# Kernel tuning notes

Measured on AMD Instinct MI355X. Metric: run time of the kernel, lower is better.

The kernel has to match this reference:

```python
import jax, jax.numpy as jnp
import numpy as np

N_NODES = 50000
N_EDGES = 800000
IN_DIM = 128
HID = 256
NUM_GRAPHS = 128


def setup_inputs() -> dict:
    key = jax.random.key(0)
    ks = jax.random.split(key, 12)
    x = jax.random.normal(ks[0], (N_NODES, IN_DIM), dtype=jnp.float32)
    edge_index = jax.random.randint(ks[1], (2, N_EDGES), 0, N_NODES, dtype=jnp.int32)
    batch = jnp.sort(jax.random.randint(ks[2], (N_NODES,), 0, NUM_GRAPHS, dtype=jnp.int32))
    def glorot(k, fan_in, fan_out):
        s = jnp.sqrt(6.0 / (fan_in + fan_out))
        return jax.random.uniform(k, (fan_in, fan_out), jnp.float32, -s, s)
    W1 = glorot(ks[3], IN_DIM, HID); b1 = jnp.zeros((HID,), jnp.float32)
    W2 = glorot(ks[4], HID, HID);    b2 = jnp.zeros((HID,), jnp.float32)
    W3 = glorot(ks[5], HID, HID // 2); b3 = jnp.zeros((HID // 2,), jnp.float32)
    W4 = glorot(ks[6], HID // 2, 1);   b4 = jnp.zeros((1,), jnp.float32)
    return {"x": x, "edge_index": edge_index, "batch": batch,
            "W1": W1, "b1": b1, "W2": W2, "b2": b2,
            "W3": W3, "b3": b3, "W4": W4, "b4": b4}


def _gcn_conv(x, src, dst, dinv, W, b, n_nodes):
    # x: [N, F_in] -> [N, F_out]; PyG GCNConv: xW gathered at src, scaled by
    # symmetric norm deg^-1/2[src]*deg^-1/2[dst], scatter-added at dst, + bias.
    h = x @ W                                   # [N, F_out]
    norm = dinv[src] * dinv[dst]                # [E+N]
    msg = h[src] * norm[:, None]                # [E+N, F_out]
    return jax.ops.segment_sum(msg, dst, num_segments=n_nodes) + b


def reference(x, edge_index, batch, W1, b1, W2, b2, W3, b3, W4, b4):
    n = x.shape[0]
    loop = jnp.arange(n, dtype=edge_index.dtype)
    src = jnp.concatenate([edge_index[0], loop])   # add self-loops
    dst = jnp.concatenate([edge_index[1], loop])
    deg = jax.ops.segment_sum(jnp.ones(src.shape[0], x.dtype), dst, num_segments=n)
    dinv = jnp.where(deg > 0, jax.lax.rsqrt(jnp.maximum(deg, 1.0)), 0.0)

    h1 = jax.nn.relu(_gcn_conv(x, src, dst, dinv, W1, b1, n))
    h2 = jax.nn.relu(_gcn_conv(h1, src, dst, dinv, W2, b2, n))

    # global_mean_pool over graph ids
    sums = jax.ops.segment_sum(h2, batch, num_segments=NUM_GRAPHS)          # [G, H]
    cnts = jax.ops.segment_sum(jnp.ones(n, h2.dtype), batch, num_segments=NUM_GRAPHS)
    g = sums / jnp.maximum(cnts, 1.0)[:, None]

    # classifier: Linear->ReLU->(Dropout eval=identity)->Linear->Sigmoid
    z = jax.nn.relu(g @ W3 + b3)
    return jax.nn.sigmoid(z @ W4 + b4)            # [G, 1]
```

## Files before the change

### kernel.cpp

```cpp
#include <hip/hip_runtime.h>
#include <math.h>

#define HID 256
#define INDIM 128
#define NPASS 8

typedef short s16x8 __attribute__((ext_vector_type(8)));
typedef float f32x4 __attribute__((ext_vector_type(4)));
typedef float f32x2 __attribute__((ext_vector_type(2)));

static __device__ __forceinline__ unsigned short f2bf(float f) {
    unsigned int u = __float_as_uint(f);
    unsigned int r = (u + 0x7fffu + ((u >> 16) & 1u)) >> 16;
    return (unsigned short)r;
}

#define DECW(a, base, w)                                                  \
    do {                                                                  \
        f32x2 p0 = __builtin_amdgcn_cvt_pk_f32_fp8((int)(w), false);      \
        f32x2 p1 = __builtin_amdgcn_cvt_pk_f32_fp8((int)(w), true);       \
        a[(base) + 0] += p0[0]; a[(base) + 1] += p0[1];                   \
        a[(base) + 2] += p1[0]; a[(base) + 3] += p1[1];                   \
    } while (0)
#define DEC16(a, u)                                                       \
    do { DECW(a, 0, (u).x); DECW(a, 4, (u).y);                            \
         DECW(a, 8, (u).z); DECW(a, 12, (u).w); } while (0)

__global__ void k_count(const int* __restrict__ dst, int E, int* cnt) {
    int e = blockIdx.x * blockDim.x + threadIdx.x;
    if (e < E) atomicAdd(&cnt[dst[e]], 1);
}

__global__ __launch_bounds__(256) void k_scan_block(const int* __restrict__ cnt,
                                                    int* excl_tmp, int* blksum, int n) {
    __shared__ int sm[256];
    int t = threadIdx.x;
    int i = blockIdx.x * 256 + t;
    int c = (i < n) ? cnt[i] : 0;
    sm[t] = c;
    __syncthreads();
    for (int off = 1; off < 256; off <<= 1) {
        int v = (t >= off) ? sm[t - off] : 0;
        __syncthreads();
        sm[t] += v;
        __syncthreads();
    }
    if (i < n) excl_tmp[i] = sm[t] - c;
    if (t == 255) blksum[blockIdx.x] = sm[255];
}

__global__ __launch_bounds__(256) void k_scan_top(int* blksum, int nb) {
    __shared__ int sm[256];
    int t = threadIdx.x;
    int c = (t < nb) ? blksum[t] : 0;
    sm[t] = c;
    __syncthreads();
    for (int off = 1; off < 256; off <<= 1) {
        int v = (t >= off) ? sm[t - off] : 0;
        __syncthreads();
        sm[t] += v;
        __syncthreads();
    }
    if (t < nb) blksum[t] = sm[t] - c;
}

__global__ __launch_bounds__(256) void k_finalize_rows(const int* __restrict__ excl_tmp,
                                                       const int* __restrict__ blksum,
                                                       const int* __restrict__ cnt,
                                                       int* row_start, int* cursor,
                                                       float* dinv, int n, int E) {
    int i = blockIdx.x * 256 + threadIdx.x;
    if (i < n) {
        int r = excl_tmp[i] + blksum[blockIdx.x];
        row_start[i] = r;
        cursor[i] = r;
        dinv[i] = rsqrtf((float)(cnt[i] + 1));
    }
    if (i == 0) row_start[n] = E;
}

__global__ void k_fill(const int* __restrict__ src, const int* __restrict__ dst,
                       int E, int* cursor, int* __restrict__ csr_src, int n) {
    int e0 = blockIdx.x * blockDim.x + threadIdx.x;
    int stride = gridDim.x * blockDim.x;
    int range = (n + NPASS - 1) / NPASS;
#pragma unroll 1
    for (int p = 0; p < NPASS; p++) {
        int lo = p * range;
        int hi = lo + range;
        for (int e = e0; e < E; e += stride) {
            int d = dst[e];
            if (d >= lo && d < hi) {
                int pos = atomicAdd(&cursor[d], 1);
                csr_src[pos] = src[e];
            }
        }
    }
}

__global__ void k_cast_q(const float* __restrict__ x, const float* __restrict__ dinv,
                         unsigned int* __restrict__ out, int nw) {
    int i = blockIdx.x * blockDim.x + threadIdx.x;
    if (i < nw) {
        float dv = dinv[i >> 5];
        float4 v = ((const float4*)x)[i];
        int w0 = __builtin_amdgcn_cvt_pk_fp8_f32(v.x * dv, v.y * dv, 0, false);
        w0 = __builtin_amdgcn_cvt_pk_fp8_f32(v.z * dv, v.w * dv, w0, true);
        out[i] = (unsigned int)w0;
    }
}

template <int K>
__global__ void k_wt(const float* __restrict__ W, unsigned short* __restrict__ Wt) {
    int c = blockIdx.x;
    int t = threadIdx.x;
    Wt[(size_t)c * K + t] = f2bf(W[(size_t)t * HID + c]);
}

template <int K, int EPI>
__global__ __launch_bounds__(256) void k_gemm_mfma(const unsigned short* __restrict__ Xb,
                                                   const unsigned short* __restrict__ Wt,
                                                   const float* __restrict__ epi,
                                                   void* __restrict__ Yout, int n) {
    constexpr int NK = K / 32;
    const int r0 = blockIdx.x * 32;
    const int w = threadIdx.x >> 6;
    const int lane = threadIdx.x & 63;
    const int ar = lane & 15;
    const int ak = (lane >> 4) * 8;

    int arow[2];
#pragma unroll
    for (int rt = 0; rt < 2; rt++) {
        int r = r0 + rt * 16 + ar;
        arow[rt] = (r < n) ? r : n - 1;
    }
    const unsigned short* Bbase = Wt + (size_t)(w * 64 + ar) * K + ak;

    s16x8 areg[2][NK];
#pragma unroll
    for (int rt = 0; rt < 2; rt++)
#pragma unroll
        for (int kk = 0; kk < NK; kk++)
            areg[rt][kk] = *(const s16x8*)(Xb + (size_t)arow[rt] * K + kk * 32);

    s16x8 breg[4][NK];
#pragma unroll
    for (int ct = 0; ct < 4; ct++)
#pragma unroll
        for (int kk = 0; kk < NK; kk++)
            breg[ct][kk] = *(const s16x8*)(Bbase + (size_t)ct * 16 * K + kk * 32);

    f32x4 acc[2][4];
#pragma unroll
    for (int rt = 0; rt < 2; rt++)
#pragma unroll
        for (int ct = 0; ct < 4; ct++) acc[rt][ct] = f32x4{0, 0, 0, 0};

#pragma unroll
    for (int kk = 0; kk < NK; kk++)
#pragma unroll
        for (int rt = 0; rt < 2; rt++)
#pragma unroll
            for (int ct = 0; ct < 4; ct++)
                acc[rt][ct] = __builtin_amdgcn_mfma_f32_16x16x32_bf16(areg[rt][kk], breg[ct][kk],
                                                                      acc[rt][ct], 0, 0, 0);

#pragma unroll
    for (int rt = 0; rt < 2; rt++) {
        int rbase = r0 + rt * 16 + (lane >> 4) * 4;
        if constexpr (EPI == 1) {
            unsigned short* Yb = (unsigned short*)Yout;
#pragma unroll
            for (int ct = 0; ct < 4; ct++) {
                int c = w * 64 + ct * 16 + ar;
                float bc = epi[c];
#pragma unroll
                for (int j = 0; j < 4; j++) {
                    int r = rbase + j;
                    if (r < n) Yb[(size_t)r * HID + c] = f2bf(fmaxf(acc[rt][ct][j] + bc, 0.0f));
                }
            }
        } else {
            unsigned char* Yq = (unsigned char*)Yout;
            float dv[4];
#pragma unroll
            for (int j = 0; j < 4; j++) dv[j] = (rbase + j < n) ? epi[rbase + j] : 0.0f;
#pragma unroll
            for (int ct = 0; ct < 4; ct++) {
                int c = w * 64 + ct * 16 + ar;
#pragma unroll
                for (int j = 0; j < 4; j++) {
                    int r = rbase + j;
                    if (r < n) {
                        float f = acc[rt][ct][j] * dv[j];
                        int e = __builtin_amdgcn_cvt_pk_fp8_f32(f, f, 0, false);
                        Yq[(size_t)r * HID + c] = (unsigned char)(e & 0xff);
                    }
                }
            }
        }
    }
}

template <int D, bool BIASRELU>
__global__ __launch_bounds__(256) void k_agg_q(const unsigned char* __restrict__ Hq,
                                               const float* __restrict__ dinv,
                                               const int* __restrict__ row_start,
                                               const int* __restrict__ csr_src,
                                               const float* __restrict__ bias,
                                               unsigned short* __restrict__ O, int n) {
    constexpr int LPR = D / 16;
    constexpr int EPW = 64 / LPR;
    const int v = blockIdx.x * 4 + (threadIdx.x >> 6);
    const int lane = threadIdx.x & 63;
    const int sub = lane / LPR;
    const int li = lane % LPR;
    if (v >= n) return;
    const uint4* H4 = (const uint4*)Hq;
    float a[16];
#pragma unroll
    for (int k = 0; k < 16; k++) a[k] = 0.f;
    const int beg = row_start[v], end = row_start[v + 1];
    int i = beg + sub;
    for (; i + 3 * EPW < end; i += 4 * EPW) {
        int s0 = csr_src[i];
        int s1 = csr_src[i + EPW];
        int s2 = csr_src[i + 2 * EPW];
        int s3 = csr_src[i + 3 * EPW];
        uint4 u0 = H4[(size_t)s0 * LPR + li];
        uint4 u1 = H4[(size_t)s1 * LPR + li];
        uint4 u2 = H4[(size_t)s2 * LPR + li];
        uint4 u3 = H4[(size_t)s3 * LPR + li];
        DEC16(a, u0); DEC16(a, u1); DEC16(a, u2); DEC16(a, u3);
    }
    for (; i < end; i += EPW) {
        uint4 u = H4[(size_t)csr_src[i] * LPR + li];
        DEC16(a, u);
    }
#pragma unroll
    for (int off = LPR; off < 64; off <<= 1)
#pragma unroll
        for (int k = 0; k < 16; k++) a[k] += __shfl_xor(a[k], off);

    if (lane < LPR) {
        uint4 us = H4[(size_t)v * LPR + li];
        DEC16(a, us);
        float dv = dinv[v];
        float o[16];
        if constexpr (BIASRELU) {
            const float4* B4 = (const float4*)bias;
#pragma unroll
            for (int q = 0; q < 4; q++) {
                float4 bb = B4[li * 4 + q];
                o[q * 4 + 0] = fmaxf(fmaf(dv, a[q * 4 + 0], bb.x), 0.f);
                o[q * 4 + 1] = fmaxf(fmaf(dv, a[q * 4 + 1], bb.y), 0.f);
                o[q * 4 + 2] = fmaxf(fmaf(dv, a[q * 4 + 2], bb.z), 0.f);
                o[q * 4 + 3] = fmaxf(fmaf(dv, a[q * 4 + 3], bb.w), 0.f);
            }
        } else {
#pragma unroll
            for (int k = 0; k < 16; k++) o[k] = dv * a[k];
        }
        uint4 ow0, ow1;
        ow0.x = (unsigned int)f2bf(o[0]) | ((unsigned int)f2bf(o[1]) << 16);
        ow0.y = (unsigned int)f2bf(o[2]) | ((unsigned int)f2bf(o[3]) << 16);
        ow0.z = (unsigned int)f2bf(o[4]) | ((unsigned int)f2bf(o[5]) << 16);
        ow0.w = (unsigned int)f2bf(o[6]) | ((unsigned int)f2bf(o[7]) << 16);
        ow1.x = (unsigned int)f2bf(o[8]) | ((unsigned int)f2bf(o[9]) << 16);
        ow1.y = (unsigned int)f2bf(o[10]) | ((unsigned int)f2bf(o[11]) << 16);
        ow1.z = (unsigned int)f2bf(o[12]) | ((unsigned int)f2bf(o[13]) << 16);
        ow1.w = (unsigned int)f2bf(o[14]) | ((unsigned int)f2bf(o[15]) << 16);
        uint4* Op = (uint4*)O + (size_t)v * (2 * LPR) + li * 2;
        Op[0] = ow0;
        Op[1] = ow1;
    }
}

#define BFLO(x) __uint_as_float((x) << 16)
#define BFHI(x) __uint_as_float((x) & 0xffff0000u)
#define ACC8(a, u)                                  \
    do {                                            \
        a[0] += BFLO((u).x); a[1] += BFHI((u).x);   \
        a[2] += BFLO((u).y); a[3] += BFHI((u).y);   \
        a[4] += BFLO((u).z); a[5] += BFHI((u).z);   \
        a[6] += BFLO((u).w); a[7] += BFHI((u).w);   \
    } while (0)

__global__ __launch_bounds__(256) void k_pool(const unsigned short* __restrict__ Hb,
                                              const int* __restrict__ batch,
                                              int n, float* __restrict__ G) {
    int g = blockIdx.x;
    int w = threadIdx.x >> 6;
    int lane = threadIdx.x & 63;
    int sub = lane >> 5;
    int li = lane & 31;
    int lo = 0, hi = n;
    while (lo < hi) { int m = (lo + hi) >> 1; if (batch[m] < g) lo = m + 1; else hi = m; }
    int start = lo;
    hi = n;
    while (lo < hi) { int m = (lo + hi) >> 1; if (batch[m] <= g) lo = m + 1; else hi = m; }
    int end = lo;
    const uint4* H4 = (const uint4*)Hb;
    float a[8] = {0, 0, 0, 0, 0, 0, 0, 0};
    for (int v = start + w * 2 + sub; v < end; v += 8) {
        uint4 u = H4[(size_t)v * 32 + li];
        ACC8(a, u);
    }
#pragma unroll
    for (int k = 0; k < 8; k++) a[k] += __shfl_xor(a[k], 32);
    __shared__ float red[4][32][8];
    if (lane < 32) {
#pragma unroll
        for (int k = 0; k < 8; k++) red[w][li][k] = a[k];
    }
    __syncthreads();
    if (w == 0 && lane < 32) {
        float inv = 1.0f / fmaxf((float)(end - start), 1.0f);
        float o[8];
#pragma unroll
        for (int k = 0; k < 8; k++)
            o[k] = (red[0][li][k] + red[1][li][k] + red[2][li][k] + red[3][li][k]) * inv;
        float4* Gp = (float4*)(G + (size_t)g * HID + li * 8);
        Gp[0] = make_float4(o[0], o[1], o[2], o[3]);
        Gp[1] = make_float4(o[4], o[5], o[6], o[7]);
    }
}

__global__ __launch_bounds__(128) void k_cls(const float* __restrict__ G,
                                             const float* __restrict__ W3,
                                             const float* __restrict__ b3,
                                             const float* __restrict__ W4,
                                             const float* __restrict__ b4,
                                             float* __restrict__ out) {
    __shared__ float gr[256];
    __shared__ float red[2];
    int g = blockIdx.x, t = threadIdx.x;
    gr[t] = G[g * 256 + t];
    gr[t + 128] = G[g * 256 + t + 128];
    __syncthreads();
    float z = b3[t];
    for (int k = 0; k < 256; k++) z += gr[k] * W3[k * 128 + t];
    z = fmaxf(z, 0.0f);
    float p = z * W4[t];
    for (int off = 32; off; off >>= 1) p += __shfl_down(p, off);
    if ((t & 63) == 0) red[t >> 6] = p;
    __syncthreads();
    if (t == 0) {
        float tot = red[0] + red[1] + b4[0];
        out[g] = 1.0f / (1.0f + expf(-tot));
    }
}

extern "C" void kernel_launch(void* const* d_in, const int* in_sizes, int n_in,
                              void* d_out, int out_size, void* d_ws, size_t ws_size,
                              hipStream_t stream) {
    const float* x  = (const float*)d_in[0];
    const int*   ei = (const int*)d_in[1];
    const int*   batch = (const int*)d_in[2];
    const float* W1 = (const float*)d_in[3];
    const float* b1 = (const float*)d_in[4];
    const float* W2 = (const float*)d_in[5];
    const float* b2 = (const float*)d_in[6];
    const float* W3 = (const float*)d_in[7];
    const float* b3 = (const float*)d_in[8];
    const float* W4 = (const float*)d_in[9];
    const float* b4 = (const float*)d_in[10];

    const int N = in_sizes[2];
    const int E = in_sizes[1] / 2;
    const int G = out_size;
    const int NB = (N + 255) / 256;

    char* w = (char*)d_ws;
    float* dinv      = (float*)w;  w += ((size_t)N * 4 + 255) & ~(size_t)255;
    int*   cnt       = (int*)w;    w += ((size_t)N * 4 + 255) & ~(size_t)255;
    int*   excl_tmp  = (int*)w;    w += ((size_t)N * 4 + 255) & ~(size_t)255;
    int*   blksum    = (int*)w;    w += 256 * 4;
    int*   row_start = (int*)w;    w += ((size_t)(N + 1) * 4 + 255) & ~(size_t)255;
    int*   cursor    = (int*)w;    w += ((size_t)N * 4 + 255) & ~(size_t)255;
    int*   csr_src   = (int*)w;    w += ((size_t)E * 4 + 255) & ~(size_t)255;
    unsigned char*  xq   = (unsigned char*)w;   w += ((size_t)N * INDIM + 255) & ~(size_t)255;
    unsigned char*  Hq   = (unsigned char*)w;   w += ((size_t)N * HID + 255) & ~(size_t)255;
    unsigned short* w1t  = (unsigned short*)w;  w += ((size_t)INDIM * HID * 2 + 255) & ~(size_t)255;
    unsigned short* w2t  = (unsigned short*)w;  w += ((size_t)HID * HID * 2 + 255) & ~(size_t)255;
    unsigned short* bufA = (unsigned short*)w;  w += (size_t)N * INDIM * 2;
    unsigned short* bufB = (unsigned short*)w;  w += (size_t)N * HID * 2;
    float* gbuf      = (float*)w;  w += (size_t)G * HID * 4;

    const int* src = ei;
    const int* dst = ei + E;

    k_wt<INDIM><<<HID, INDIM, 0, stream>>>(W1, w1t);
    k_wt<HID><<<HID, HID, 0, stream>>>(W2, w2t);

    hipMemsetAsync(cnt, 0, (size_t)N * 4, stream);
    k_count<<<(E + 255) / 256, 256, 0, stream>>>(dst, E, cnt);
    k_scan_block<<<NB, 256, 0, stream>>>(cnt, excl_tmp, blksum, N);
    k_scan_top<<<1, 256, 0, stream>>>(blksum, NB);
    k_finalize_rows<<<NB, 256, 0, stream>>>(excl_tmp, blksum, cnt, row_start, cursor, dinv, N, E);
    k_fill<<<(E + 255) / 256, 256, 0, stream>>>(src, dst, E, cursor, csr_src, N);

    int nw = N * INDIM / 4;
    k_cast_q<<<(nw + 255) / 256, 256, 0, stream>>>(x, dinv, (unsigned int*)xq, nw);

    const int gemm_blocks = (N + 31) / 32;
    const int agg_blocks  = (N + 3) / 4;

    k_agg_q<INDIM, false><<<agg_blocks, 256, 0, stream>>>(xq, dinv, row_start, csr_src, nullptr, bufA, N);
    k_gemm_mfma<INDIM, 1><<<gemm_blocks, 256, 0, stream>>>(bufA, w1t, b1, bufB, N);

    k_gemm_mfma<HID, 2><<<gemm_blocks, 256, 0, stream>>>(bufB, w2t, dinv, Hq, N);
    k_agg_q<HID, true><<<agg_blocks, 256, 0, stream>>>(Hq, dinv, row_start, csr_src, b2, bufB, N);

    k_pool<<<G, 256, 0, stream>>>(bufB, batch, N, gbuf);
    k_cls<<<G, 128, 0, stream>>>(gbuf, W3, b3, W4, b4, (float*)d_out);
}
```

Measured before the change: 296.7 us.

## Stage pre-swizzled weight fragments in LDS and retile GEMM blocks by column

Weights are now pre-packed into the MFMA fragment layout. Each GEMM block loads its 64-column slice of that layout into shared memory once, so waves no longer each fetch a full weight slice from global memory into registers. Blocks now cover 128 rows by 64 columns, with each wave handling 32 rows, and A fragments are prefetched one k-step ahead instead of all being held in registers. This lowers register pressure and repeated weight traffic, but adds LDS staging and a barrier, and each A row is now read by four column blocks.

New measurement: 272.2 us. 8.3% less time.

```diff
diff --git a/kernel.cpp b/kernel.cpp
--- a/kernel.cpp
+++ b/kernel.cpp
@@ -111,69 +111,94 @@
 }
 
 template <int K>
-__global__ void k_wt(const float* __restrict__ W, unsigned short* __restrict__ Wt) {
-    int c = blockIdx.x;
-    int t = threadIdx.x;
-    Wt[(size_t)c * K + t] = f2bf(W[(size_t)t * HID + c]);
+__global__ void k_wtf(const float* __restrict__ W, uint4* __restrict__ Wfrag) {
+    constexpr int NK = K / 32;
+    int c_tile = blockIdx.x / NK;
+    int kk = blockIdx.x % NK;
+    int lane = threadIdx.x;
+    int c = c_tile * 16 + (lane & 15);
+    int k0 = kk * 32 + (lane >> 4) * 8;
+    unsigned short b[8];
+#pragma unroll
+    for (int j = 0; j < 8; j++) b[j] = f2bf(W[(size_t)(k0 + j) * HID + c]);
+    uint4 o;
+    o.x = (unsigned int)b[0] | ((unsigned int)b[1] << 16);
+    o.y = (unsigned int)b[2] | ((unsigned int)b[3] << 16);
+    o.z = (unsigned int)b[4] | ((unsigned int)b[5] << 16);
+    o.w = (unsigned int)b[6] | ((unsigned int)b[7] << 16);
+    Wfrag[(size_t)(c_tile * NK + kk) * 64 + lane] = o;
 }
 
 template <int K, int EPI>
 __global__ __launch_bounds__(256) void k_gemm_mfma(const unsigned short* __restrict__ Xb,
-                                                   const unsigned short* __restrict__ Wt,
+                                                   const uint4* __restrict__ Wfrag,
                                                    const float* __restrict__ epi,
                                                    void* __restrict__ Yout, int n) {
     constexpr int NK = K / 32;
-    const int r0 = blockIdx.x * 32;
+    __shared__ uint4 bl[4 * NK * 64];
+
+    const int nb = blockIdx.x & 3;
+    const int mb = blockIdx.x >> 2;
+    const int r0 = mb * 128;
     const int w = threadIdx.x >> 6;
     const int lane = threadIdx.x & 63;
     const int ar = lane & 15;
     const int ak = (lane >> 4) * 8;
 
+    {
+        const uint4* gsrc = Wfrag + (size_t)nb * 4 * NK * 64;
+        for (int i = threadIdx.x; i < 4 * NK * 64; i += 256) bl[i] = gsrc[i];
+    }
+
     int arow[2];
 #pragma unroll
     for (int rt = 0; rt < 2; rt++) {
-        int r = r0 + rt * 16 + ar;
+        int r = r0 + w * 32 + rt * 16 + ar;
         arow[rt] = (r < n) ? r : n - 1;
     }
-    const unsigned short* Bbase = Wt + (size_t)(w * 64 + ar) * K + ak;
-
-    s16x8 areg[2][NK];
+
+    f32x4 acc[2][4];
 #pragma unroll
     for (int rt = 0; rt < 2; rt++)
 #pragma unroll
-        for (int kk = 0; kk < NK; kk++)
-            areg[rt][kk] = *(const s16x8*)(Xb + (size_t)arow[rt] * K + kk * 32);
-
-    s16x8 breg[4][NK];
-#pragma unroll
-    for (int ct = 0; ct < 4; ct++)
-#pragma unroll
-        for (int kk = 0; kk < NK; kk++)
-            breg[ct][kk] = *(const s16x8*)(Bbase + (size_t)ct * 16 * K + kk * 32);
-
-    f32x4 acc[2][4];
+        for (int ct = 0; ct < 4; ct++) acc[rt][ct] = f32x4{0, 0, 0, 0};
+
+    __syncthreads();
+
+    s16x8 a_cur[2], a_nxt[2];
 #pragma unroll
     for (int rt = 0; rt < 2; rt++)
-#pragma unroll
-        for (int ct = 0; ct < 4; ct++) acc[rt][ct] = f32x4{0, 0, 0, 0};
-
-#pragma unroll
-    for (int kk = 0; kk < NK; kk++)
+        a_cur[rt] = *(const s16x8*)(Xb + (size_t)arow[rt] * K + ak);
+
+#pragma unroll
+    for (int kk = 0; kk < NK; kk++) {
+        if (kk + 1 < NK) {
+#pragma unroll
+            for (int rt = 0; rt < 2; rt++)
+                a_nxt[rt] = *(const s16x8*)(Xb + (size_t)arow[rt] * K + (kk + 1) * 32 + ak);
+        }
+        s16x8 bfrag[4];
+#pragma unroll
+        for (int ct = 0; ct < 4; ct++)
+            bfrag[ct] = ((const s16x8*)bl)[(ct * NK + kk) * 64 + lane];
 #pragma unroll
         for (int rt = 0; rt < 2; rt++)
 #pragma unroll
             for (int ct = 0; ct < 4; ct++)
-                acc[rt][ct] = __builtin_amdgcn_mfma_f32_16x16x32_bf16(areg[rt][kk], breg[ct][kk],
+                acc[rt][ct] = __builtin_amdgcn_mfma_f32_16x16x32_bf16(a_cur[rt], bfrag[ct],
                                                                       acc[rt][ct], 0, 0, 0);
+#pragma unroll
+        for (int rt = 0; rt < 2; rt++) a_cur[rt] = a_nxt[rt];
+    }
 
 #pragma unroll
     for (int rt = 0; rt < 2; rt++) {
-        int rbase = r0 + rt * 16 + (lane >> 4) * 4;
+        int rbase = r0 + w * 32 + rt * 16 + (lane >> 4) * 4;
         if constexpr (EPI == 1) {
             unsigned short* Yb = (unsigned short*)Yout;
 #pragma unroll
             for (int ct = 0; ct < 4; ct++) {
-                int c = w * 64 + ct * 16 + ar;
+                int c = nb * 64 + ct * 16 + ar;
                 float bc = epi[c];
 #pragma unroll
                 for (int j = 0; j < 4; j++) {
@@ -188,7 +213,7 @@
             for (int j = 0; j < 4; j++) dv[j] = (rbase + j < n) ? epi[rbase + j] : 0.0f;
 #pragma unroll
             for (int ct = 0; ct < 4; ct++) {
-                int c = w * 64 + ct * 16 + ar;
+                int c = nb * 64 + ct * 16 + ar;
 #pragma unroll
                 for (int j = 0; j < 4; j++) {
                     int r = rbase + j;
@@ -382,8 +407,8 @@
     int*   csr_src   = (int*)w;    w += ((size_t)E * 4 + 255) & ~(size_t)255;
     unsigned char*  xq   = (unsigned char*)w;   w += ((size_t)N * INDIM + 255) & ~(size_t)255;
     unsigned char*  Hq   = (unsigned char*)w;   w += ((size_t)N * HID + 255) & ~(size_t)255;
-    unsigned short* w1t  = (unsigned short*)w;  w += ((size_t)INDIM * HID * 2 + 255) & ~(size_t)255;
-    unsigned short* w2t  = (unsigned short*)w;  w += ((size_t)HID * HID * 2 + 255) & ~(size_t)255;
+    uint4* wf1 = (uint4*)w;  w += ((size_t)INDIM * HID * 2 + 255) & ~(size_t)255;
+    uint4* wf2 = (uint4*)w;  w += ((size_t)HID * HID * 2 + 255) & ~(size_t)255;
     unsigned short* bufA = (unsigned short*)w;  w += (size_t)N * INDIM * 2;
     unsigned short* bufB = (unsigned short*)w;  w += (size_t)N * HID * 2;
     float* gbuf      = (float*)w;  w += (size_t)G * HID * 4;
@@ -391,8 +416,8 @@
     const int* src = ei;
     const int* dst = ei + E;
 
-    k_wt<INDIM><<<HID, INDIM, 0, stream>>>(W1, w1t);
-    k_wt<HID><<<HID, HID, 0, stream>>>(W2, w2t);
+    k_wtf<INDIM><<<16 * (INDIM / 32), 64, 0, stream>>>(W1, wf1);
+    k_wtf<HID><<<16 * (HID / 32), 64, 0, stream>>>(W2, wf2);
 
     hipMemsetAsync(cnt, 0, (size_t)N * 4, stream);
     k_count<<<(E + 255) / 256, 256, 0, stream>>>(dst, E, cnt);
@@ -404,13 +429,13 @@
     int nw = N * INDIM / 4;
     k_cast_q<<<(nw + 255) / 256, 256, 0, stream>>>(x, dinv, (unsigned int*)xq, nw);
 
-    const int gemm_blocks = (N + 31) / 32;
+    const int gemm_blocks = ((N + 127) / 128) * 4;
     const int agg_blocks  = (N + 3) / 4;
 
     k_agg_q<INDIM, false><<<agg_blocks, 256, 0, stream>>>(xq, dinv, row_start, csr_src, nullptr, bufA, N);
-    k_gemm_mfma<INDIM, 1><<<gemm_blocks, 256, 0, stream>>>(bufA, w1t, b1, bufB, N);
-
-    k_gemm_mfma<HID, 2><<<gemm_blocks, 256, 0, stream>>>(bufB, w2t, dinv, Hq, N);
+    k_gemm_mfma<INDIM, 1><<<gemm_blocks, 256, 0, stream>>>(bufA, wf1, b1, bufB, N);
+
+    k_gemm_mfma<HID, 2><<<gemm_blocks, 256, 0, stream>>>(bufB, wf2, dinv, Hq, N);
     k_agg_q<HID, true><<<agg_blocks, 256, 0, stream>>>(Hq, dinv, row_start, csr_src, b2, bufB, N);
 
     k_pool<<<G, 256, 0, stream>>>(bufB, batch, N, gbuf);
```
